# Kernel optimization log

Hardware: AMD Instinct MI355X
Metric: run time of the kernel (lower is better)

Reference implementation:

```python
import jax, jax.numpy as jnp
import numpy as np

N_NODES, N_EDGES = 50000, 800000
IN_DIM, HID, LAT, HEADS = 512, 256, 64, 1
SLOPE = 0.2  # LeakyReLU negative_slope (PyG GATConv default)


def setup_inputs() -> dict:
    key = jax.random.key(0)
    ks = jax.random.split(key, 6)
    x = jax.random.normal(ks[0], (N_NODES, IN_DIM), jnp.float32)
    edge_index = jax.random.randint(ks[1], (2, N_EDGES), 0, N_NODES, jnp.int32)
    s = 0.1
    # STAGATE-style GATConv: lin_src is a raw Parameter [in, heads*out]; x_src = x_dst = x @ lin_src
    W1 = jax.random.normal(ks[2], (IN_DIM, HEADS * HID), jnp.float32) * s      # encoder_gat1.lin_src
    W2 = jax.random.normal(ks[3], (HID, HEADS * LAT), jnp.float32) * s          # encoder_gat2.lin_src
    att_src1 = jax.random.normal(ks[4], (1, HEADS, HID), jnp.float32) * s
    att_dst1 = jax.random.normal(ks[5], (1, HEADS, HID), jnp.float32) * s
    return dict(x=x, edge_index=edge_index, W1=W1, W2=W2,
                att_src1=att_src1, att_dst1=att_dst1)


def _gat_attend(h, a_src, a_dst, src, dst, n):
    """Edge attention + segment softmax over dst + scatter-add aggregation.
    h: [N,H,C]; a_src, a_dst: [N,H]. Returns head-mean output [N,C] (concat=False)."""
    e = a_src[src] + a_dst[dst]                          # [E,H] attention logits
    e = jnp.where(e > 0, e, SLOPE * e)                   # LeakyReLU
    m = jax.ops.segment_max(e, dst, num_segments=n)      # [N,H] per-dst max (stable softmax)
    ex = jnp.exp(e - m[dst])
    denom = jax.ops.segment_sum(ex, dst, num_segments=n)
    alpha = ex / denom[dst]                              # [E,H] normalized attention
    msg = h[src] * alpha[:, :, None]                     # [E,H,C] messages (dropout inactive: eval)
    out = jax.ops.segment_sum(msg, dst, num_segments=n)  # [N,H,C]
    return out.mean(axis=1)


def reference(x, edge_index, W1, W2, att_src1, att_dst1):
    n, H = x.shape[0], HEADS
    src, dst = edge_index[0], edge_index[1]
    # encoder_gat1 (attention=True); stores attentions for tying in decode
    h1 = (x @ W1).reshape(n, H, -1)                      # [N,H,HID]
    a_src1 = (h1 * att_src1).sum(-1)                     # [N,H]
    a_dst1 = (h1 * att_dst1).sum(-1)                     # [N,H]
    h1o = jax.nn.elu(_gat_attend(h1, a_src1, a_dst1, src, dst, n))
    # encoder_gat2 (attention=False): returns x_src head-mean, no propagation
    latent = (h1o @ W2).reshape(n, H, -1).mean(axis=1)   # [N,LAT]
    # decoder_gat1: lin tied to W2^T, attention tied to encoder_gat1's (a_src1, a_dst1)
    h3 = (latent @ W2.T).reshape(n, H, -1)               # [N,H,HID]
    h3o = jax.nn.relu(_gat_attend(h3, a_src1, a_dst1, src, dst, n))
    # decoder_gat2: lin tied to W1^T, attention=False
    recon = (h3o @ W1.T).reshape(n, H, -1).mean(axis=1)  # [N,IN_DIM]
    return latent, recon
```

## Files before the change

kernel.cpp:

```cpp
#include <hip/hip_runtime.h>

#define NN 50000
#define NE 800000
#define IND 512
#define HIDD 256
#define LATD 64

typedef __attribute__((ext_vector_type(8))) short bh8;
typedef __attribute__((ext_vector_type(8))) unsigned short us8;
typedef __attribute__((ext_vector_type(4))) float f4v;

__device__ __forceinline__ unsigned short f2bf(float f) {
    unsigned int x = __float_as_uint(f);
    x += 0x7fffu + ((x >> 16) & 1u);
    return (unsigned short)(x >> 16);
}

__global__ void hist_k(const int* __restrict__ ei, int* __restrict__ cnt) {
    int e = blockIdx.x * 256 + threadIdx.x;
    if (e < NE) atomicAdd(&cnt[ei[NE + e]], 1);
}

__global__ __launch_bounds__(1024) void scan_k(const int* __restrict__ cnt,
                                               int* __restrict__ row_ptr) {
    __shared__ int buf[1024];
    int tid = threadIdx.x;
    int carry = 0;
    for (int base = 0; base < NN; base += 1024) {
        int idx = base + tid;
        int v = (idx < NN) ? cnt[idx] : 0;
        buf[tid] = v;
        __syncthreads();
        for (int off = 1; off < 1024; off <<= 1) {
            int t = (tid >= off) ? buf[tid - off] : 0;
            __syncthreads();
            buf[tid] += t;
            __syncthreads();
        }
        if (idx < NN) row_ptr[idx] = carry + buf[tid] - v;
        carry += buf[1023];
        __syncthreads();
    }
    if (tid == 0) row_ptr[NN] = carry;
}

__global__ void scatter_k(const int* __restrict__ ei, const int* __restrict__ row_ptr,
                          int* __restrict__ cursor, int* __restrict__ sorted_src) {
    int e = blockIdx.x * 256 + threadIdx.x;
    if (e >= NE) return;
    int s = ei[e], d = ei[NE + e];
    int pos = row_ptr[d] + atomicAdd(&cursor[d], 1);
    sorted_src[pos] = s;
}

__global__ void wprep_k(const float* __restrict__ W1, unsigned short* __restrict__ W1bf,
                        unsigned short* __restrict__ W1T) {
    int i = blockIdx.x * 256 + threadIdx.x;
    if (i >= IND * HIDD) return;
    int k = i / HIDD, n = i % HIDD;
    unsigned short b = f2bf(W1[i]);
    W1bf[i] = b;
    W1T[n * IND + k] = b;
}

template <int BN, bool AF32>
__global__ __launch_bounds__(BN) void mfma_gemm_k(const void* __restrict__ Araw,
                                                  const unsigned short* __restrict__ Bt,
                                                  float* __restrict__ C,
                                                  int M, int K) {
    constexpr int LDP = 40;
    __shared__ unsigned short Asm[64 * LDP];
    __shared__ unsigned short Bsm[BN * LDP];

    const int tid = threadIdx.x;
    const int wave = tid >> 6;
    const int lane = tid & 63;
    const int quad = lane >> 4;
    const int l16 = lane & 15;
    const int m0 = blockIdx.y * 64;

    const float* Af = (const float*)Araw;
    const unsigned short* Abf = (const unsigned short*)Araw;

    f4v acc[4][4];
#pragma unroll
    for (int i = 0; i < 4; i++)
#pragma unroll
        for (int j = 0; j < 4; j++) acc[i][j] = (f4v)(0.f);

    for (int k0 = 0; k0 < K; k0 += 32) {
        if (AF32) {
#pragma unroll
            for (int f = tid; f < 512; f += BN) {
                int row = f >> 3, kc = (f & 7) * 4;
                int gm = m0 + row;
                float4 v = make_float4(0.f, 0.f, 0.f, 0.f);
                if (gm < M) v = *(const float4*)(Af + (size_t)gm * K + k0 + kc);
                ushort4 w;
                w.x = f2bf(v.x); w.y = f2bf(v.y); w.z = f2bf(v.z); w.w = f2bf(v.w);
                *(ushort4*)&Asm[row * LDP + kc] = w;
            }
        } else {
            if (tid < 256) {
                int row = tid >> 2, kc = (tid & 3) * 8;
                int gm = m0 + row;
                us8 v = {0, 0, 0, 0, 0, 0, 0, 0};
                if (gm < M) v = *(const us8*)(Abf + (size_t)gm * K + k0 + kc);
                *(us8*)&Asm[row * LDP + kc] = v;
            }
        }
#pragma unroll
        for (int i = 0; i < 4; i++) {
            int f = i * BN + tid;
            int r = f >> 2, kq = (f & 3) * 8;
            us8 v = *(const us8*)(Bt + (size_t)r * K + k0 + kq);
            *(us8*)&Bsm[r * LDP + kq] = v;
        }
        __syncthreads();

        bh8 a[4], b[4];
#pragma unroll
        for (int mi = 0; mi < 4; mi++)
            a[mi] = *(const bh8*)&Asm[(mi * 16 + l16) * LDP + quad * 8];
#pragma unroll
        for (int ni = 0; ni < 4; ni++)
            b[ni] = *(const bh8*)&Bsm[(wave * 64 + ni * 16 + l16) * LDP + quad * 8];
#pragma unroll
        for (int mi = 0; mi < 4; mi++)
#pragma unroll
            for (int ni = 0; ni < 4; ni++)
                acc[mi][ni] = __builtin_amdgcn_mfma_f32_16x16x32_bf16(
                    a[mi], b[ni], acc[mi][ni], 0, 0, 0);
        __syncthreads();
    }

#pragma unroll
    for (int mi = 0; mi < 4; mi++) {
        int rbase = m0 + mi * 16 + quad * 4;
#pragma unroll
        for (int ni = 0; ni < 4; ni++) {
            int gc = wave * 64 + ni * 16 + l16;
#pragma unroll
            for (int r = 0; r < 4; r++) {
                int gr = rbase + r;
                if (gr < M) C[(size_t)gr * BN + gc] = acc[mi][ni][r];
            }
        }
    }
}

template <bool TRANSB, int EPI>
__global__ __launch_bounds__(256) void gemm_k(const float* __restrict__ A,
                                              const float* __restrict__ B,
                                              float* __restrict__ C,
                                              float* __restrict__ O,
                                              int M, int N, int K, int ldb) {
    __shared__ float As[16][64];
    __shared__ float Bs[16][64];
    const int tid = threadIdx.x;
    const int tx = tid & 15, ty = tid >> 4;
    const int n0 = blockIdx.x * 64;
    const int m0 = blockIdx.y * 64;

    const int arow = tid >> 2;
    const int ak = (tid & 3) * 4;
    const int bcol = tid & 63;
    const int bk = (tid >> 6) * 4;

    float acc[4][4] = {};

    for (int k0 = 0; k0 < K; k0 += 16) {
        int gm = m0 + arow;
        if (gm < M) {
            float4 v = *(const float4*)(A + (size_t)gm * K + k0 + ak);
            As[ak + 0][arow] = v.x;
            As[ak + 1][arow] = v.y;
            As[ak + 2][arow] = v.z;
            As[ak + 3][arow] = v.w;
        } else {
            As[ak + 0][arow] = 0.f;
            As[ak + 1][arow] = 0.f;
            As[ak + 2][arow] = 0.f;
            As[ak + 3][arow] = 0.f;
        }
        if (!TRANSB) {
#pragma unroll
            for (int i = 0; i < 4; i++)
                Bs[bk + i][bcol] = B[(size_t)(k0 + bk + i) * ldb + n0 + bcol];
        } else {
            float4 v = *(const float4*)(B + (size_t)(n0 + bcol) * ldb + k0 + bk);
            Bs[bk + 0][bcol] = v.x;
            Bs[bk + 1][bcol] = v.y;
            Bs[bk + 2][bcol] = v.z;
            Bs[bk + 3][bcol] = v.w;
        }
        __syncthreads();
#pragma unroll
        for (int k = 0; k < 16; k++) {
            float4 a = *(const float4*)&As[k][ty * 4];
            float4 b = *(const float4*)&Bs[k][tx * 4];
            float av[4] = {a.x, a.y, a.z, a.w};
            float bv[4] = {b.x, b.y, b.z, b.w};
#pragma unroll
            for (int i = 0; i < 4; i++)
#pragma unroll
                for (int j = 0; j < 4; j++) acc[i][j] += av[i] * bv[j];
        }
        __syncthreads();
    }

#pragma unroll
    for (int i = 0; i < 4; i++) {
        int gm = m0 + ty * 4 + i;
        if (gm >= M) continue;
#pragma unroll
        for (int j = 0; j < 4; j++) {
            int gn = n0 + tx * 4 + j;
            float v = acc[i][j];
            C[(size_t)gm * N + gn] = v;
            if (EPI == 1) O[(size_t)gm * N + gn] = v;
        }
    }
}

__global__ __launch_bounds__(256) void rowdots_k(const float* __restrict__ h1,
                                                 const float* __restrict__ att_s,
                                                 const float* __restrict__ att_d,
                                                 float* __restrict__ a_src,
                                                 float* __restrict__ a_dst) {
    int wave = threadIdx.x >> 6, lane = threadIdx.x & 63;
    int node = blockIdx.x * 4 + wave;
    if (node >= NN) return;
    int c = lane * 4;
    float4 h = *(const float4*)&h1[(size_t)node * HIDD + c];
    float4 s4 = *(const float4*)&att_s[c];
    float4 d4 = *(const float4*)&att_d[c];
    float ps = h.x * s4.x + h.y * s4.y + h.z * s4.z + h.w * s4.w;
    float pd = h.x * d4.x + h.y * d4.y + h.z * d4.z + h.w * d4.w;
    for (int off = 32; off; off >>= 1) {
        ps += __shfl_down(ps, off, 64);
        pd += __shfl_down(pd, off, 64);
    }
    if (lane == 0) {
        a_src[node] = ps;
        a_dst[node] = pd;
    }
}

__global__ __launch_bounds__(256) void attend1_k(const int* __restrict__ row_ptr,
                                                 const int* __restrict__ sorted_src,
                                                 const float* __restrict__ a_src,
                                                 const float* __restrict__ a_dst,
                                                 const float* __restrict__ h1,
                                                 float* __restrict__ alpha,
                                                 float* __restrict__ h1o) {
    int wave = threadIdx.x >> 6, lane = threadIdx.x & 63;
    int d = blockIdx.x * 4 + wave;
    if (d >= NN) return;
    int beg = row_ptr[d], end = row_ptr[d + 1];
    int deg = end - beg;
    float ad = a_dst[d];

    float lm = -3.0e38f;
    for (int t = lane; t < deg; t += 64) {
        int s = sorted_src[beg + t];
        float e = a_src[s] + ad;
        e = e > 0.f ? e : 0.2f * e;
        lm = fmaxf(lm, e);
    }
    for (int off = 32; off; off >>= 1) lm = fmaxf(lm, __shfl_down(lm, off, 64));
    lm = __shfl(lm, 0, 64);

    float ls = 0.f;
    for (int t = lane; t < deg; t += 64) {
        int s = sorted_src[beg + t];
        float e = a_src[s] + ad;
        e = e > 0.f ? e : 0.2f * e;
        ls += expf(e - lm);
    }
    for (int off = 32; off; off >>= 1) ls += __shfl_down(ls, off, 64);
    ls = __shfl(ls, 0, 64);
    float inv = (deg > 0) ? 1.f / ls : 0.f;

    int c = lane * 4;
    float4 acc = make_float4(0.f, 0.f, 0.f, 0.f);
    for (int t = 0; t < deg; t++) {
        int s = sorted_src[beg + t];
        float e = a_src[s] + ad;
        e = e > 0.f ? e : 0.2f * e;
        float al = expf(e - lm) * inv;
        if (lane == 0) alpha[beg + t] = al;
        float4 h = *(const float4*)&h1[(size_t)s * HIDD + c];
        acc.x += al * h.x;
        acc.y += al * h.y;
        acc.z += al * h.z;
        acc.w += al * h.w;
    }
    acc.x = acc.x > 0.f ? acc.x : expm1f(acc.x);
    acc.y = acc.y > 0.f ? acc.y : expm1f(acc.y);
    acc.z = acc.z > 0.f ? acc.z : expm1f(acc.z);
    acc.w = acc.w > 0.f ? acc.w : expm1f(acc.w);
    *(float4*)&h1o[(size_t)d * HIDD + c] = acc;
}

__global__ __launch_bounds__(256) void attend2_k(const int* __restrict__ row_ptr,
                                                 const int* __restrict__ sorted_src,
                                                 const float* __restrict__ alpha,
                                                 const float* __restrict__ h3,
                                                 unsigned short* __restrict__ h3bf) {
    int wave = threadIdx.x >> 6, lane = threadIdx.x & 63;
    int d = blockIdx.x * 4 + wave;
    if (d >= NN) return;
    int beg = row_ptr[d], end = row_ptr[d + 1];
    int deg = end - beg;
    int c = lane * 4;
    float4 acc = make_float4(0.f, 0.f, 0.f, 0.f);
    for (int t = 0; t < deg; t++) {
        float al = alpha[beg + t];
        int s = sorted_src[beg + t];
        float4 h = *(const float4*)&h3[(size_t)s * HIDD + c];
        acc.x += al * h.x;
        acc.y += al * h.y;
        acc.z += al * h.z;
        acc.w += al * h.w;
    }
    ushort4 o;
    o.x = f2bf(fmaxf(acc.x, 0.f));
    o.y = f2bf(fmaxf(acc.y, 0.f));
    o.z = f2bf(fmaxf(acc.z, 0.f));
    o.w = f2bf(fmaxf(acc.w, 0.f));
    *(ushort4*)&h3bf[(size_t)d * HIDD + c] = o;
}

extern "C" void kernel_launch(void* const* d_in, const int* in_sizes, int n_in,
                              void* d_out, int out_size, void* d_ws, size_t ws_size,
                              hipStream_t stream) {
    const float* x = (const float*)d_in[0];
    const int* ei = (const int*)d_in[1];
    const float* W1 = (const float*)d_in[2];
    const float* W2 = (const float*)d_in[3];
    const float* att_s = (const float*)d_in[4];
    const float* att_d = (const float*)d_in[5];
    float* out_lat = (float*)d_out;
    float* out_rec = out_lat + (size_t)NN * LATD;

    char* ws = (char*)d_ws;
    size_t off = 0;
    auto alloc = [&](size_t bytes) -> void* {
        void* p = ws + off;
        off += (bytes + 255) & ~(size_t)255;
        return p;
    };
    float* bufA = (float*)alloc((size_t)NN * HIDD * 4);
    float* bufB = (float*)alloc((size_t)NN * HIDD * 4);
    float* lat = (float*)alloc((size_t)NN * LATD * 4);
    float* a_src = (float*)alloc((size_t)NN * 4);
    float* a_dst = (float*)alloc((size_t)NN * 4);
    float* alpha = (float*)alloc((size_t)NE * 4);
    int* cnt = (int*)alloc((size_t)NN * 4);
    int* cursor = (int*)alloc((size_t)NN * 4);
    int* row_ptr = (int*)alloc((size_t)(NN + 1) * 4);
    int* sorted = (int*)alloc((size_t)NE * 4);
    unsigned short* W1bf = (unsigned short*)alloc((size_t)IND * HIDD * 2);
    unsigned short* W1T = (unsigned short*)alloc((size_t)IND * HIDD * 2);
    unsigned short* h3bf = (unsigned short*)bufB;

    hipMemsetAsync(cnt, 0, (size_t)NN * 4, stream);
    hipMemsetAsync(cursor, 0, (size_t)NN * 4, stream);

    const int EB = (NE + 255) / 256;
    const int NB4 = (NN + 3) / 4;
    const int MB = (NN + 63) / 64;

    wprep_k<<<(IND * HIDD + 255) / 256, 256, 0, stream>>>(W1, W1bf, W1T);
    hist_k<<<EB, 256, 0, stream>>>(ei, cnt);
    scan_k<<<1, 1024, 0, stream>>>(cnt, row_ptr);
    scatter_k<<<EB, 256, 0, stream>>>(ei, row_ptr, cursor, sorted);

    mfma_gemm_k<HIDD, true><<<dim3(1, MB), HIDD, 0, stream>>>(
        (const void*)x, W1T, bufA, NN, IND);

    rowdots_k<<<NB4, 256, 0, stream>>>(bufA, att_s, att_d, a_src, a_dst);
    attend1_k<<<NB4, 256, 0, stream>>>(row_ptr, sorted, a_src, a_dst, bufA, alpha, bufB);

    gemm_k<false, 1><<<dim3(LATD / 64, MB), 256, 0, stream>>>(
        bufB, W2, lat, out_lat, NN, LATD, HIDD, LATD);

    gemm_k<true, 0><<<dim3(HIDD / 64, MB), 256, 0, stream>>>(
        lat, W2, bufA, nullptr, NN, HIDD, LATD, LATD);

    attend2_k<<<NB4, 256, 0, stream>>>(row_ptr, sorted, alpha, bufA, h3bf);

    mfma_gemm_k<IND, false><<<dim3(1, MB), IND, 0, stream>>>(
        (const void*)h3bf, W1bf, out_rec, NN, HIDD);
}
```

Measured before the change: 739.4 us.

## Store h1 and h3 intermediates in bf16 and unroll gather loops by four

The first GEMM and the h3 GEMM now write bf16 outputs instead of fp32, halving the bytes read by the random-gather aggregation in both attention kernels and by rowdots. The attention kernels unroll the neighbour loop by four so more gathers are in flight at once. attend1 now writes alpha in parallel across lanes instead of from lane 0 inside the serial loop, and uses fast __expf. Rounding intermediates to bf16 adds precision loss in the attention logits and aggregated features.

```diff
diff --git a/kernel.cpp b/kernel.cpp
--- a/kernel.cpp
+++ b/kernel.cpp
@@ -14,6 +14,9 @@
     unsigned int x = __float_as_uint(f);
     x += 0x7fffu + ((x >> 16) & 1u);
     return (unsigned short)(x >> 16);
+}
+__device__ __forceinline__ float bf2f(unsigned short u) {
+    return __uint_as_float(((unsigned int)u) << 16);
 }
 
 __global__ void hist_k(const int* __restrict__ ei, int* __restrict__ cnt) {
@@ -63,10 +66,10 @@
     W1T[n * IND + k] = b;
 }
 
-template <int BN, bool AF32>
+template <int BN, bool AF32, bool CBF16>
 __global__ __launch_bounds__(BN) void mfma_gemm_k(const void* __restrict__ Araw,
                                                   const unsigned short* __restrict__ Bt,
-                                                  float* __restrict__ C,
+                                                  void* __restrict__ Cout,
                                                   int M, int K) {
     constexpr int LDP = 40;
     __shared__ unsigned short Asm[64 * LDP];
@@ -143,7 +146,12 @@
 #pragma unroll
             for (int r = 0; r < 4; r++) {
                 int gr = rbase + r;
-                if (gr < M) C[(size_t)gr * BN + gc] = acc[mi][ni][r];
+                if (gr < M) {
+                    if (CBF16)
+                        ((unsigned short*)Cout)[(size_t)gr * BN + gc] = f2bf(acc[mi][ni][r]);
+                    else
+                        ((float*)Cout)[(size_t)gr * BN + gc] = acc[mi][ni][r];
+                }
             }
         }
     }
@@ -154,6 +162,7 @@
                                               const float* __restrict__ B,
                                               float* __restrict__ C,
                                               float* __restrict__ O,
+                                              unsigned short* __restrict__ Obf,
                                               int M, int N, int K, int ldb) {
     __shared__ float As[16][64];
     __shared__ float Bs[16][64];
@@ -217,13 +226,19 @@
         for (int j = 0; j < 4; j++) {
             int gn = n0 + tx * 4 + j;
             float v = acc[i][j];
-            C[(size_t)gm * N + gn] = v;
-            if (EPI == 1) O[(size_t)gm * N + gn] = v;
-        }
-    }
-}
-
-__global__ __launch_bounds__(256) void rowdots_k(const float* __restrict__ h1,
+            if (EPI == 0) {
+                C[(size_t)gm * N + gn] = v;
+            } else if (EPI == 1) {
+                C[(size_t)gm * N + gn] = v;
+                O[(size_t)gm * N + gn] = v;
+            } else {
+                Obf[(size_t)gm * N + gn] = f2bf(v);
+            }
+        }
+    }
+}
+
+__global__ __launch_bounds__(256) void rowdots_k(const unsigned short* __restrict__ h1bf,
                                                  const float* __restrict__ att_s,
                                                  const float* __restrict__ att_d,
                                                  float* __restrict__ a_src,
@@ -232,11 +247,12 @@
     int node = blockIdx.x * 4 + wave;
     if (node >= NN) return;
     int c = lane * 4;
-    float4 h = *(const float4*)&h1[(size_t)node * HIDD + c];
+    ushort4 hu = *(const ushort4*)&h1bf[(size_t)node * HIDD + c];
     float4 s4 = *(const float4*)&att_s[c];
     float4 d4 = *(const float4*)&att_d[c];
-    float ps = h.x * s4.x + h.y * s4.y + h.z * s4.z + h.w * s4.w;
-    float pd = h.x * d4.x + h.y * d4.y + h.z * d4.z + h.w * d4.w;
+    float hx = bf2f(hu.x), hy = bf2f(hu.y), hz = bf2f(hu.z), hw = bf2f(hu.w);
+    float ps = hx * s4.x + hy * s4.y + hz * s4.z + hw * s4.w;
+    float pd = hx * d4.x + hy * d4.y + hz * d4.z + hw * d4.w;
     for (int off = 32; off; off >>= 1) {
         ps += __shfl_down(ps, off, 64);
         pd += __shfl_down(pd, off, 64);
@@ -246,12 +262,14 @@
         a_dst[node] = pd;
     }
 }
+
+__device__ __forceinline__ float lrelu(float e) { return e > 0.f ? e : 0.2f * e; }
 
 __global__ __launch_bounds__(256) void attend1_k(const int* __restrict__ row_ptr,
                                                  const int* __restrict__ sorted_src,
                                                  const float* __restrict__ a_src,
                                                  const float* __restrict__ a_dst,
-                                                 const float* __restrict__ h1,
+                                                 const unsigned short* __restrict__ h1bf,
                                                  float* __restrict__ alpha,
                                                  float* __restrict__ h1o) {
     int wave = threadIdx.x >> 6, lane = threadIdx.x & 63;
@@ -264,37 +282,57 @@
     float lm = -3.0e38f;
     for (int t = lane; t < deg; t += 64) {
         int s = sorted_src[beg + t];
-        float e = a_src[s] + ad;
-        e = e > 0.f ? e : 0.2f * e;
-        lm = fmaxf(lm, e);
+        lm = fmaxf(lm, lrelu(a_src[s] + ad));
     }
     for (int off = 32; off; off >>= 1) lm = fmaxf(lm, __shfl_down(lm, off, 64));
     lm = __shfl(lm, 0, 64);
 
-    float ls = 0.f;
+    float ls = 0.f, ex0 = 0.f;
     for (int t = lane; t < deg; t += 64) {
         int s = sorted_src[beg + t];
-        float e = a_src[s] + ad;
-        e = e > 0.f ? e : 0.2f * e;
-        ls += expf(e - lm);
+        float ex = __expf(lrelu(a_src[s] + ad) - lm);
+        if (t == lane) ex0 = ex;
+        ls += ex;
     }
     for (int off = 32; off; off >>= 1) ls += __shfl_down(ls, off, 64);
     ls = __shfl(ls, 0, 64);
     float inv = (deg > 0) ? 1.f / ls : 0.f;
 
+    if (lane < deg) alpha[beg + lane] = ex0 * inv;
+    for (int t = lane + 64; t < deg; t += 64) {
+        int s = sorted_src[beg + t];
+        alpha[beg + t] = __expf(lrelu(a_src[s] + ad) - lm) * inv;
+    }
+
     int c = lane * 4;
     float4 acc = make_float4(0.f, 0.f, 0.f, 0.f);
-    for (int t = 0; t < deg; t++) {
+    int t = 0;
+    for (; t + 4 <= deg; t += 4) {
+        int s0 = sorted_src[beg + t + 0];
+        int s1 = sorted_src[beg + t + 1];
+        int s2 = sorted_src[beg + t + 2];
+        int s3 = sorted_src[beg + t + 3];
+        ushort4 h0 = *(const ushort4*)&h1bf[(size_t)s0 * HIDD + c];
+        ushort4 h1v = *(const ushort4*)&h1bf[(size_t)s1 * HIDD + c];
+        ushort4 h2 = *(const ushort4*)&h1bf[(size_t)s2 * HIDD + c];
+        ushort4 h3 = *(const ushort4*)&h1bf[(size_t)s3 * HIDD + c];
+        float a0 = __expf(lrelu(a_src[s0] + ad) - lm) * inv;
+        float a1 = __expf(lrelu(a_src[s1] + ad) - lm) * inv;
+        float a2 = __expf(lrelu(a_src[s2] + ad) - lm) * inv;
+        float a3 = __expf(lrelu(a_src[s3] + ad) - lm) * inv;
+        acc.x += a0 * bf2f(h0.x) + a1 * bf2f(h1v.x) + a2 * bf2f(h2.x) + a3 * bf2f(h3.x);
+        acc.y += a0 * bf2f(h0.y) + a1 * bf2f(h1v.y) + a2 * bf2f(h2.y) + a3 * bf2f(h3.y);
+        acc.z += a0 * bf2f(h0.z) + a1 * bf2f(h1v.z) + a2 * bf2f(h2.z) + a3 * bf2f(h3.z);
+        acc.w += a0 * bf2f(h0.w) + a1 * bf2f(h1v.w) + a2 * bf2f(h2.w) + a3 * bf2f(h3.w);
+    }
+    for (; t < deg; t++) {
         int s = sorted_src[beg + t];
-        float e = a_src[s] + ad;
-        e = e > 0.f ? e : 0.2f * e;
-        float al = expf(e - lm) * inv;
-        if (lane == 0) alpha[beg + t] = al;
-        float4 h = *(const float4*)&h1[(size_t)s * HIDD + c];
-        acc.x += al * h.x;
-        acc.y += al * h.y;
-        acc.z += al * h.z;
-        acc.w += al * h.w;
+        float al = __expf(lrelu(a_src[s] + ad) - lm) * inv;
+        ushort4 h = *(const ushort4*)&h1bf[(size_t)s * HIDD + c];
+        acc.x += al * bf2f(h.x);
+        acc.y += al * bf2f(h.y);
+        acc.z += al * bf2f(h.z);
+        acc.w += al * bf2f(h.w);
     }
     acc.x = acc.x > 0.f ? acc.x : expm1f(acc.x);
     acc.y = acc.y > 0.f ? acc.y : expm1f(acc.y);
@@ -306,8 +344,8 @@
 __global__ __launch_bounds__(256) void attend2_k(const int* __restrict__ row_ptr,
                                                  const int* __restrict__ sorted_src,
                                                  const float* __restrict__ alpha,
-                                                 const float* __restrict__ h3,
-                                                 unsigned short* __restrict__ h3bf) {
+                                                 const unsigned short* __restrict__ h3bf,
+                                                 unsigned short* __restrict__ h3obf) {
     int wave = threadIdx.x >> 6, lane = threadIdx.x & 63;
     int d = blockIdx.x * 4 + wave;
     if (d >= NN) return;
@@ -315,21 +353,40 @@
     int deg = end - beg;
     int c = lane * 4;
     float4 acc = make_float4(0.f, 0.f, 0.f, 0.f);
-    for (int t = 0; t < deg; t++) {
+    int t = 0;
+    for (; t + 4 <= deg; t += 4) {
+        int s0 = sorted_src[beg + t + 0];
+        int s1 = sorted_src[beg + t + 1];
+        int s2 = sorted_src[beg + t + 2];
+        int s3 = sorted_src[beg + t + 3];
+        float a0 = alpha[beg + t + 0];
+        float a1 = alpha[beg + t + 1];
+        float a2 = alpha[beg + t + 2];
+        float a3 = alpha[beg + t + 3];
+        ushort4 h0 = *(const ushort4*)&h3bf[(size_t)s0 * HIDD + c];
+        ushort4 h1v = *(const ushort4*)&h3bf[(size_t)s1 * HIDD + c];
+        ushort4 h2 = *(const ushort4*)&h3bf[(size_t)s2 * HIDD + c];
+        ushort4 h3 = *(const ushort4*)&h3bf[(size_t)s3 * HIDD + c];
+        acc.x += a0 * bf2f(h0.x) + a1 * bf2f(h1v.x) + a2 * bf2f(h2.x) + a3 * bf2f(h3.x);
+        acc.y += a0 * bf2f(h0.y) + a1 * bf2f(h1v.y) + a2 * bf2f(h2.y) + a3 * bf2f(h3.y);
+        acc.z += a0 * bf2f(h0.z) + a1 * bf2f(h1v.z) + a2 * bf2f(h2.z) + a3 * bf2f(h3.z);
+        acc.w += a0 * bf2f(h0.w) + a1 * bf2f(h1v.w) + a2 * bf2f(h2.w) + a3 * bf2f(h3.w);
+    }
+    for (; t < deg; t++) {
         float al = alpha[beg + t];
         int s = sorted_src[beg + t];
-        float4 h = *(const float4*)&h3[(size_t)s * HIDD + c];
-        acc.x += al * h.x;
-        acc.y += al * h.y;
-        acc.z += al * h.z;
-        acc.w += al * h.w;
+        ushort4 h = *(const ushort4*)&h3bf[(size_t)s * HIDD + c];
+        acc.x += al * bf2f(h.x);
+        acc.y += al * bf2f(h.y);
+        acc.z += al * bf2f(h.z);
+        acc.w += al * bf2f(h.w);
     }
     ushort4 o;
     o.x = f2bf(fmaxf(acc.x, 0.f));
     o.y = f2bf(fmaxf(acc.y, 0.f));
     o.z = f2bf(fmaxf(acc.z, 0.f));
     o.w = f2bf(fmaxf(acc.w, 0.f));
-    *(ushort4*)&h3bf[(size_t)d * HIDD + c] = o;
+    *(ushort4*)&h3obf[(size_t)d * HIDD + c] = o;
 }
 
 extern "C" void kernel_launch(void* const* d_in, const int* in_sizes, int n_in,
@@ -351,7 +408,7 @@
         off += (bytes + 255) & ~(size_t)255;
         return p;
     };
-    float* bufA = (float*)alloc((size_t)NN * HIDD * 4);
+    unsigned short* h1bf = (unsigned short*)alloc((size_t)NN * HIDD * 2);
     float* bufB = (float*)alloc((size_t)NN * HIDD * 4);
     float* lat = (float*)alloc((size_t)NN * LATD * 4);
     float* a_src = (float*)alloc((size_t)NN * 4);
@@ -363,7 +420,8 @@
     int* sorted = (int*)alloc((size_t)NE * 4);
     unsigned short* W1bf = (unsigned short*)alloc((size_t)IND * HIDD * 2);
     unsigned short* W1T = (unsigned short*)alloc((size_t)IND * HIDD * 2);
-    unsigned short* h3bf = (unsigned short*)bufB;
+    unsigned short* h3bf = h1bf;
+    unsigned short* h3obf = (unsigned short*)bufB;
 
     hipMemsetAsync(cnt, 0, (size_t)NN * 4, stream);
     hipMemsetAsync(cursor, 0, (size_t)NN * 4, stream);
@@ -377,20 +435,20 @@
     scan_k<<<1, 1024, 0, stream>>>(cnt, row_ptr);
     scatter_k<<<EB, 256, 0, stream>>>(ei, row_ptr, cursor, sorted);
 
-    mfma_gemm_k<HIDD, true><<<dim3(1, MB), HIDD, 0, stream>>>(
-        (const void*)x, W1T, bufA, NN, IND);
-
-    rowdots_k<<<NB4, 256, 0, stream>>>(bufA, att_s, att_d, a_src, a_dst);
-    attend1_k<<<NB4, 256, 0, stream>>>(row_ptr, sorted, a_src, a_dst, bufA, alpha, bufB);
+    mfma_gemm_k<HIDD, true, true><<<dim3(1, MB), HIDD, 0, stream>>>(
+        (const void*)x, W1T, (void*)h1bf, NN, IND);
+
+    rowdots_k<<<NB4, 256, 0, stream>>>(h1bf, att_s, att_d, a_src, a_dst);
+    attend1_k<<<NB4, 256, 0, stream>>>(row_ptr, sorted, a_src, a_dst, h1bf, alpha, bufB);
 
     gemm_k<false, 1><<<dim3(LATD / 64, MB), 256, 0, stream>>>(
-        bufB, W2, lat, out_lat, NN, LATD, HIDD, LATD);
-
-    gemm_k<true, 0><<<dim3(HIDD / 64, MB), 256, 0, stream>>>(
-        lat, W2, bufA, nullptr, NN, HIDD, LATD, LATD);
-
-    attend2_k<<<NB4, 256, 0, stream>>>(row_ptr, sorted, alpha, bufA, h3bf);
-
-    mfma_gemm_k<IND, false><<<dim3(1, MB), IND, 0, stream>>>(
-        (const void*)h3bf, W1bf, out_rec, NN, HIDD);
-}
+        bufB, W2, lat, out_lat, nullptr, NN, LATD, HIDD, LATD);
+
+    gemm_k<true, 2><<<dim3(HIDD / 64, MB), 256, 0, stream>>>(
+        lat, W2, nullptr, nullptr, h3bf, NN, HIDD, LATD, LATD);
+
+    attend2_k<<<NB4, 256, 0, stream>>>(row_ptr, sorted, alpha, h3bf, h3obf);
+
+    mfma_gemm_k<IND, false, false><<<dim3(1, MB), IND, 0, stream>>>(
+        (const void*)h3obf, W1bf, (void*)out_rec, NN, HIDD);
+}
```

New measurement: 627.8 us. -15.1%, faster.
